# Performance work log

Hardware: AMD Instinct MI355X
Metric: run time of the kernel (lower is better)

Reference implementation:

```python
import jax, jax.numpy as jnp
import numpy as np

B, L, D, DIN, A, V, R = 1024, 100, 256, 704, 128, 32000, 129


def setup_inputs() -> dict:
    key = jax.random.key(0)
    ks = jax.random.split(key, 18)
    s = 0.05
    inp = {
        "x": jax.random.normal(ks[0], (B, DIN), jnp.float32),
        "h0": jax.random.normal(ks[1], (B, D), jnp.float32),
        "c0": jax.random.normal(ks[2], (B, D), jnp.float32),
        "src_enc": jax.random.normal(ks[3], (B, L, D), jnp.float32),
        "src_token_ids": jax.random.randint(ks[4], (B, L), 0, V),
        "W_ih": jax.random.normal(ks[5], (4 * D, DIN), jnp.float32) * s,
        "b_ih": jax.random.normal(ks[6], (4 * D,), jnp.float32) * s,
        "W_hh": jax.random.normal(ks[7], (4 * D, D), jnp.float32) * s,
        "b_hh": jax.random.normal(ks[8], (4 * D,), jnp.float32) * s,
        "W_attn": jax.random.normal(ks[9], (D, D), jnp.float32) * s,
        "W_att_vec": jax.random.normal(ks[10], (A * 2, 2 * D), jnp.float32) * s,
        "W_ptr": jax.random.normal(ks[11], (D, D), jnp.float32) * s,
        "rule_emb": jax.random.normal(ks[12], (R, 128), jnp.float32) * s,
        "W_rule_proj": jax.random.normal(ks[13], (D, 128), jnp.float32) * s,
        "prim_emb": jax.random.normal(ks[14], (V, 128), jnp.float32) * s,
        "W_prim_proj": jax.random.normal(ks[15], (D, 128), jnp.float32) * s,
        "w_gen": jax.random.normal(ks[16], (2, D), jnp.float32) * s,
        "b_gen": jax.random.normal(ks[17], (2,), jnp.float32) * s,
    }
    # W_att_vec maps concat(h, ctx) [2D] -> ATT (=256); keep shape (256, 512)
    inp["W_att_vec"] = inp["W_att_vec"][:256]
    return inp


def reference(x, h0, c0, src_enc, src_token_ids, W_ih, b_ih, W_hh, b_hh,
              W_attn, W_att_vec, W_ptr, rule_emb, W_rule_proj,
              prim_emb, W_prim_proj, w_gen, b_gen):
    # --- LSTMCell (torch gate order i, f, g, o) ---
    gates = x @ W_ih.T + b_ih + h0 @ W_hh.T + b_hh          # [B, 4D]
    i, f, g, o = jnp.split(gates, 4, axis=-1)
    i, f, o = jax.nn.sigmoid(i), jax.nn.sigmoid(f), jax.nn.sigmoid(o)
    c = f * c0 + i * jnp.tanh(g)
    h = o * jnp.tanh(c)                                      # [B, D]

    # --- dot-product attention over source encodings ---
    enc_proj = src_enc @ W_attn.T                            # [B, L, D]
    scores = jnp.einsum('bd,bld->bl', h, enc_proj)
    alpha = jax.nn.softmax(scores, axis=-1)
    ctx = jnp.einsum('bl,bld->bd', alpha, src_enc)
    att = jnp.tanh(jnp.concatenate([h, ctx], axis=-1) @ W_att_vec.T)  # [B, 256]

    # --- apply-rule (production) readout ---
    rule_proj = rule_emb @ W_rule_proj.T                     # [R, 256]
    log_p_rule = jax.nn.log_softmax(att @ rule_proj.T, axis=-1)  # [B, R]

    # --- primitive generation readout ---
    prim_proj = prim_emb @ W_prim_proj.T                     # [V, 256]
    p_gen_prim = jax.nn.softmax(att @ prim_proj.T, axis=-1)  # [B, V]

    # --- pointer network copy distribution over source positions ---
    ptr_scores = jnp.einsum('bld,bd->bl', src_enc @ W_ptr.T, att)
    copy_p = jax.nn.softmax(ptr_scores, axis=-1)             # [B, L]

    # --- gen vs copy gate (softmax over 2, per usage in parse()) ---
    gate = jax.nn.softmax(att @ w_gen.T + b_gen, axis=-1)    # [B, 2]

    # --- combined primitive distribution: gen + scattered copy mass ---
    p_prim = gate[:, :1] * p_gen_prim                        # [B, V]
    copy_mass = gate[:, 1:] * copy_p                         # [B, L]
    bidx = jnp.arange(p_prim.shape[0])[:, None]
    p_prim = p_prim.at[bidx, src_token_ids].add(copy_mass)
    return log_p_rule, p_prim, h, c, att
```

## Files before the change

kernel.cpp:

```cpp
#include <hip/hip_runtime.h>
#include <hip/hip_bf16.h>
#include <math.h>

#define NB   1024
#define LL   100
#define DD   256
#define DINN 704
#define VV   32000
#define RR   129
#define KAV  512
#define ROWU 129

typedef float f32x4 __attribute__((ext_vector_type(4)));
typedef float f32x2 __attribute__((ext_vector_type(2)));
typedef short s16x8 __attribute__((ext_vector_type(8)));
typedef unsigned short u16;
typedef unsigned int u32;

__device__ __forceinline__ float sigf(float x) { return 1.0f / (1.0f + __expf(-x)); }

__device__ __forceinline__ u16 f2bf(float f) {
    u32 u = __float_as_uint(f);
    u += 0x7fffu + ((u >> 16) & 1u);
    return (u16)(u >> 16);
}
__device__ __forceinline__ float bf2f(u16 s) {
    return __uint_as_float(((u32)s) << 16);
}

__global__ __launch_bounds__(256) void k_conv(
    const float* __restrict__ prim_emb, u16* __restrict__ prim_bf,
    const float* __restrict__ W_ih, u16* __restrict__ wih_bf,
    const float* __restrict__ W_hh, u16* __restrict__ whh_bf,
    const float* __restrict__ x, u16* __restrict__ x_bf,
    const float* __restrict__ h0, u16* __restrict__ h0_bf,
    const float* __restrict__ rule_emb, const float* __restrict__ W_rule_proj,
    float* __restrict__ rpT)
{
    __shared__ float re_s[128];
    const int bx = blockIdx.x, t = threadIdx.x;

    const float* src; u16* dst; int off;
    if (bx < 2000)      { src = prim_emb; dst = prim_bf; off = bx * 2048; }
    else if (bx < 2352) { src = W_ih;  dst = wih_bf; off = (bx - 2000) * 2048; }
    else if (bx < 2480) { src = W_hh;  dst = whh_bf; off = (bx - 2352) * 2048; }
    else if (bx < 2832) { src = x;     dst = x_bf;   off = (bx - 2480) * 2048; }
    else                { src = h0;    dst = h0_bf;  off = (bx - 2832) * 2048; }

    if (bx < RR && t < 128) re_s[t] = rule_emb[bx * 128 + t];

    int i = off + t * 8;
    f32x4 a = *reinterpret_cast<const f32x4*>(&src[i]);
    f32x4 b = *reinterpret_cast<const f32x4*>(&src[i + 4]);
    s16x8 r;
    r[0] = (short)f2bf(a[0]); r[1] = (short)f2bf(a[1]);
    r[2] = (short)f2bf(a[2]); r[3] = (short)f2bf(a[3]);
    r[4] = (short)f2bf(b[0]); r[5] = (short)f2bf(b[1]);
    r[6] = (short)f2bf(b[2]); r[7] = (short)f2bf(b[3]);
    *reinterpret_cast<s16x8*>(&dst[i]) = r;

    if (bx < RR) {
        __syncthreads();
        float acc = 0.f;
        const float* __restrict__ wr = &W_rule_proj[t * 128];
#pragma unroll 8
        for (int k = 0; k < 128; k += 4) {
            f32x4 w4 = *reinterpret_cast<const f32x4*>(&wr[k]);
            acc += w4[0] * re_s[k] + w4[1] * re_s[k + 1]
                 + w4[2] * re_s[k + 2] + w4[3] * re_s[k + 3];
        }
        rpT[t * 192 + bx] = acc;
    }
}

__global__ __launch_bounds__(256) void k_lstm(
    const u16* __restrict__ x_bf, const u16* __restrict__ h0_bf,
    const float* __restrict__ c0,
    const u16* __restrict__ wih_bf, const u16* __restrict__ whh_bf,
    const float* __restrict__ b_ih, const float* __restrict__ b_hh,
    float* __restrict__ out_h, float* __restrict__ out_c)
{
    const int t = threadIdx.x;
    const int lane = t & 63, w = t >> 6;
    const int lm = lane & 15, lq = lane >> 4;
    const int dg = blockIdx.x;
    const int row0 = blockIdx.y * 128 + w * 32;
    f32x4 acc[4][2] = {};

    for (int kt = 0; kt < 22; ++kt) {
        const int ko = kt * 32 + lq * 8;
        s16x8 bfr[4], afr[2];
#pragma unroll
        for (int mg = 0; mg < 4; ++mg)
            bfr[mg] = *reinterpret_cast<const s16x8*>(
                &wih_bf[(mg * 256 + dg * 16 + lm) * DINN + ko]);
#pragma unroll
        for (int ng = 0; ng < 2; ++ng)
            afr[ng] = *reinterpret_cast<const s16x8*>(
                &x_bf[(row0 + ng * 16 + lm) * DINN + ko]);
#pragma unroll
        for (int mg = 0; mg < 4; ++mg)
#pragma unroll
            for (int ng = 0; ng < 2; ++ng)
                acc[mg][ng] = __builtin_amdgcn_mfma_f32_16x16x32_bf16(
                    bfr[mg], afr[ng], acc[mg][ng], 0, 0, 0);
    }
    for (int kt = 0; kt < 8; ++kt) {
        const int ko = kt * 32 + lq * 8;
        s16x8 bfr[4], afr[2];
#pragma unroll
        for (int mg = 0; mg < 4; ++mg)
            bfr[mg] = *reinterpret_cast<const s16x8*>(
                &whh_bf[(mg * 256 + dg * 16 + lm) * DD + ko]);
#pragma unroll
        for (int ng = 0; ng < 2; ++ng)
            afr[ng] = *reinterpret_cast<const s16x8*>(
                &h0_bf[(row0 + ng * 16 + lm) * DD + ko]);
#pragma unroll
        for (int mg = 0; mg < 4; ++mg)
#pragma unroll
            for (int ng = 0; ng < 2; ++ng)
                acc[mg][ng] = __builtin_amdgcn_mfma_f32_16x16x32_bf16(
                    bfr[mg], afr[ng], acc[mg][ng], 0, 0, 0);
    }

    const int dc = dg * 16 + lq * 4;
    f32x4 bi[4];
#pragma unroll
    for (int mg = 0; mg < 4; ++mg) {
        f32x4 a4 = *reinterpret_cast<const f32x4*>(&b_ih[mg * 256 + dc]);
        f32x4 b4 = *reinterpret_cast<const f32x4*>(&b_hh[mg * 256 + dc]);
        bi[mg][0] = a4[0] + b4[0]; bi[mg][1] = a4[1] + b4[1];
        bi[mg][2] = a4[2] + b4[2]; bi[mg][3] = a4[3] + b4[3];
    }
#pragma unroll
    for (int ng = 0; ng < 2; ++ng) {
        const int row = row0 + ng * 16 + lm;
        f32x4 c4 = *reinterpret_cast<const f32x4*>(&c0[row * DD + dc]);
        f32x4 h4, cc4;
#pragma unroll
        for (int r = 0; r < 4; ++r) {
            float iv = acc[0][ng][r] + bi[0][r];
            float fv = acc[1][ng][r] + bi[1][r];
            float gv = acc[2][ng][r] + bi[2][r];
            float ov = acc[3][ng][r] + bi[3][r];
            float cc = sigf(fv) * c4[r] + sigf(iv) * tanhf(gv);
            cc4[r] = cc;
            h4[r] = sigf(ov) * tanhf(cc);
        }
        *reinterpret_cast<f32x4*>(&out_c[row * DD + dc]) = cc4;
        *reinterpret_cast<f32x4*>(&out_h[row * DD + dc]) = h4;
    }
}

__global__ __launch_bounds__(256) void k_hw(
    const float* __restrict__ h, const float* __restrict__ W_attn, float* __restrict__ hW)
{
    __shared__ __align__(16) float As[16][36];
    __shared__ __align__(16) float Bs[16][68];
    const int t = threadIdx.x;
    const int row0 = blockIdx.x * 32;
    const int col0 = blockIdx.y * 64;
    const int tr = t >> 4, tc = t & 15;
    float acc[2][4] = {};
    for (int kt = 0; kt < 16; ++kt) {
        __syncthreads();
#pragma unroll
        for (int p = 0; p < 2; ++p) {
            int e = t + p * 256;
            int r = e >> 4, kk = e & 15;
            As[kk][r] = h[(row0 + r) * DD + kt * 16 + kk];
        }
#pragma unroll
        for (int p = 0; p < 4; ++p) {
            int e = t + p * 256;
            int kk = e >> 6, c = e & 63;
            Bs[kk][c] = W_attn[(kt * 16 + kk) * DD + col0 + c];
        }
        __syncthreads();
#pragma unroll
        for (int kk = 0; kk < 16; ++kk) {
            float a0 = As[kk][tr * 2], a1 = As[kk][tr * 2 + 1];
            f32x4 b = *reinterpret_cast<const f32x4*>(&Bs[kk][tc * 4]);
#pragma unroll
            for (int i = 0; i < 4; ++i) {
                acc[0][i] = fmaf(a0, b[i], acc[0][i]);
                acc[1][i] = fmaf(a1, b[i], acc[1][i]);
            }
        }
    }
#pragma unroll
    for (int j = 0; j < 2; ++j) {
        f32x4 v;
#pragma unroll
        for (int i = 0; i < 4; ++i) v[i] = acc[j][i];
        *reinterpret_cast<f32x4*>(&hW[(row0 + tr * 2 + j) * DD + col0 + tc * 4]) = v;
    }
}

__global__ __launch_bounds__(256, 2) void k_attn2(
    const float* __restrict__ src_enc, const float* __restrict__ hW,
    float* __restrict__ ctx_out)
{
    __shared__ u32 enc_u[LL * ROWU];
    __shared__ __align__(16) float part[4][DD];
    __shared__ __align__(16) float hw_s[DD];
    __shared__ float sc_s[LL];
    __shared__ float al_s[LL];

    const int b = blockIdx.x, t = threadIdx.x;
    const int lane = t & 63, w = t >> 6;
    const float* __restrict__ enc = src_enc + (size_t)b * LL * DD;

    hw_s[t] = hW[b * DD + t];

#pragma unroll
    for (int p = 0; p < 25; ++p) {
        int q = p * 256 + t;
        int l = q >> 6, dq = q & 63;
        f32x4 ev = *reinterpret_cast<const f32x4*>(&enc[l * DD + dq * 4]);
        u32 w0 = (u32)f2bf(ev[0]) | ((u32)f2bf(ev[1]) << 16);
        u32 w1 = (u32)f2bf(ev[2]) | ((u32)f2bf(ev[3]) << 16);
        enc_u[l * ROWU + dq * 2]     = w0;
        enc_u[l * ROWU + dq * 2 + 1] = w1;
    }
    __syncthreads();

    {
        const int sl = ((w >> 1) << 6) + lane;
        float sp = 0.f;
        if (sl < LL) {
            const u32* __restrict__ rp = enc_u + sl * ROWU + ((w & 1) << 6);
            const float* __restrict__ hp = hw_s + ((w & 1) << 7);
#pragma unroll 32
            for (int k = 0; k < 64; ++k) {
                u32 v = rp[k];
                sp = fmaf(bf2f((u16)v),         hp[2 * k],     sp);
                sp = fmaf(bf2f((u16)(v >> 16)), hp[2 * k + 1], sp);
            }
        }
        part[w][lane] = sp;
    }
    __syncthreads();
    if (t < LL) sc_s[t] = part[(t >> 6) << 1][t & 63] + part[((t >> 6) << 1) + 1][t & 63];
    __syncthreads();

    if (w == 0) {
        float v0 = sc_s[lane];
        float v1 = (lane + 64 < LL) ? sc_s[lane + 64] : -1e30f;
        float m = fmaxf(v0, v1);
#pragma unroll
        for (int s = 1; s < 64; s <<= 1) m = fmaxf(m, __shfl_xor(m, s));
        float e0 = __expf(v0 - m);
        float e1 = (lane + 64 < LL) ? __expf(v1 - m) : 0.f;
        float ssum = e0 + e1;
#pragma unroll
        for (int s = 1; s < 64; s <<= 1) ssum += __shfl_xor(ssum, s);
        float inv = 1.f / ssum;
        al_s[lane] = e0 * inv;
        if (lane + 64 < LL) al_s[lane + 64] = e1 * inv;
    }
    __syncthreads();

    {
        const int l0 = w * 25;
        float c0 = 0.f, c1 = 0.f, c2 = 0.f, c3 = 0.f;
#pragma unroll
        for (int li = 0; li < 25; ++li) {
            int l = l0 + li;
            float a = al_s[l];
            u32 v0 = enc_u[l * ROWU + lane * 2];
            u32 v1 = enc_u[l * ROWU + lane * 2 + 1];
            c0 = fmaf(a, bf2f((u16)v0), c0);
            c1 = fmaf(a, bf2f((u16)(v0 >> 16)), c1);
            c2 = fmaf(a, bf2f((u16)v1), c2);
            c3 = fmaf(a, bf2f((u16)(v1 >> 16)), c3);
        }
        f32x4 p; p[0] = c0; p[1] = c1; p[2] = c2; p[3] = c3;
        *reinterpret_cast<f32x4*>(&part[w][lane * 4]) = p;
    }
    __syncthreads();
    ctx_out[b * DD + t] = (part[0][t] + part[1][t]) + (part[2][t] + part[3][t]);
}

__global__ __launch_bounds__(256) void k_att(
    const float* __restrict__ h, const float* __restrict__ ctx,
    const float* __restrict__ W_att_vec, float* __restrict__ att_out)
{
    __shared__ __align__(16) float As[16][36];
    __shared__ __align__(16) float Bs[16][68];
    const int t = threadIdx.x;
    const int row0 = blockIdx.x * 32;
    const int col0 = blockIdx.y * 64;
    const int tr = t >> 4, tc = t & 15;
    float acc[2][4] = {};
    for (int kt = 0; kt < 32; ++kt) {
        const float* __restrict__ Asrc = (kt < 16) ? h : ctx;
        int kb = (kt < 16) ? kt * 16 : (kt - 16) * 16;
        int kg = kt * 16;
        __syncthreads();
#pragma unroll
        for (int p = 0; p < 2; ++p) {
            int e = t + p * 256;
            int r = e >> 4, kk = e & 15;
            As[kk][r] = Asrc[(row0 + r) * DD + kb + kk];
        }
#pragma unroll
        for (int p = 0; p < 4; ++p) {
            int e = t + p * 256;
            int r = e >> 4, kk = e & 15;
            Bs[kk][r] = W_att_vec[(col0 + r) * KAV + kg + kk];
        }
        __syncthreads();
#pragma unroll
        for (int kk = 0; kk < 16; ++kk) {
            float a0 = As[kk][tr * 2], a1 = As[kk][tr * 2 + 1];
            f32x4 b = *reinterpret_cast<const f32x4*>(&Bs[kk][tc * 4]);
#pragma unroll
            for (int i = 0; i < 4; ++i) {
                acc[0][i] = fmaf(a0, b[i], acc[0][i]);
                acc[1][i] = fmaf(a1, b[i], acc[1][i]);
            }
        }
    }
#pragma unroll
    for (int j = 0; j < 2; ++j)
#pragma unroll
        for (int i = 0; i < 4; ++i)
            att_out[(row0 + tr * 2 + j) * DD + col0 + tc * 4 + i] = tanhf(acc[j][i]);
}

__global__ __launch_bounds__(256) void k_ptrproj(
    const float* __restrict__ att, const float* __restrict__ W_ptr,
    const float* __restrict__ W_prim_proj, const float* __restrict__ rpT,
    float* __restrict__ atw, u16* __restrict__ att_bf, float* __restrict__ rl)
{
    __shared__ __align__(16) float As[16][36];
    __shared__ __align__(16) float Bs[16][68];
    const int t = threadIdx.x;
    const int row0 = blockIdx.x * 32;
    const int col0 = blockIdx.y * 64;
    const int tr = t >> 4, tc = t & 15;
    float acc[2][4] = {};
    for (int kt = 0; kt < 16; ++kt) {
        __syncthreads();
#pragma unroll
        for (int p = 0; p < 2; ++p) {
            int e = t + p * 256;
            int r = e >> 4, kk = e & 15;
            As[kk][r] = att[(row0 + r) * DD + kt * 16 + kk];
        }
#pragma unroll
        for (int p = 0; p < 4; ++p) {
            int e = t + p * 256;
            int kk = e >> 6, c = e & 63;
            float bv;
            if (col0 < 256)      bv = W_ptr[(kt * 16 + kk) * DD + col0 + c];
            else if (col0 < 384) bv = W_prim_proj[(kt * 16 + kk) * 128 + (col0 - 256) + c];
            else {
                int rc = col0 - 384 + c;
                bv = (rc < RR) ? rpT[(kt * 16 + kk) * 192 + rc] : 0.f;
            }
            Bs[kk][c] = bv;
        }
        __syncthreads();
#pragma unroll
        for (int kk = 0; kk < 16; ++kk) {
            float a0 = As[kk][tr * 2], a1 = As[kk][tr * 2 + 1];
            f32x4 b = *reinterpret_cast<const f32x4*>(&Bs[kk][tc * 4]);
#pragma unroll
            for (int i = 0; i < 4; ++i) {
                acc[0][i] = fmaf(a0, b[i], acc[0][i]);
                acc[1][i] = fmaf(a1, b[i], acc[1][i]);
            }
        }
    }
    if (col0 < 256) {
#pragma unroll
        for (int j = 0; j < 2; ++j) {
            f32x4 v;
#pragma unroll
            for (int i = 0; i < 4; ++i) v[i] = acc[j][i];
            *reinterpret_cast<f32x4*>(&atw[(row0 + tr * 2 + j) * DD + col0 + tc * 4]) = v;
        }
    } else if (col0 < 384) {
#pragma unroll
        for (int j = 0; j < 2; ++j)
#pragma unroll
            for (int i = 0; i < 4; ++i)
                att_bf[(row0 + tr * 2 + j) * 128 + (col0 - 256) + tc * 4 + i] = f2bf(acc[j][i]);
    } else {
#pragma unroll
        for (int j = 0; j < 2; ++j)
#pragma unroll
            for (int i = 0; i < 4; ++i) {
                int rc = col0 - 384 + tc * 4 + i;
                if (rc < RR) rl[(row0 + tr * 2 + j) * 132 + rc] = acc[j][i];
            }
    }
}

__global__ __launch_bounds__(256) void k_fin(
    const float* __restrict__ rl, const float* __restrict__ att,
    const float* __restrict__ w_gen, const float* __restrict__ b_gen,
    float* __restrict__ log_p_rule, float* __restrict__ gate0_ws,
    float* __restrict__ gate1_ws)
{
    const int w = threadIdx.x >> 6, lane = threadIdx.x & 63;
    const int b = blockIdx.x * 4 + w;

    float v0 = rl[b * 132 + lane];
    float v1 = rl[b * 132 + 64 + lane];
    float v2 = (lane == 0) ? rl[b * 132 + 128] : -1e30f;
    float m = fmaxf(fmaxf(v0, v1), v2);
#pragma unroll
    for (int s = 1; s < 64; s <<= 1) m = fmaxf(m, __shfl_xor(m, s));
    float ssum = __expf(v0 - m) + __expf(v1 - m) + ((lane == 0) ? __expf(v2 - m) : 0.f);
#pragma unroll
    for (int s = 1; s < 64; s <<= 1) ssum += __shfl_xor(ssum, s);
    float ls = m + logf(ssum);
    log_p_rule[b * RR + lane] = v0 - ls;
    log_p_rule[b * RR + 64 + lane] = v1 - ls;
    if (lane == 0) log_p_rule[b * RR + 128] = v2 - ls;

    f32x4 a4 = *reinterpret_cast<const f32x4*>(&att[b * DD + lane * 4]);
    f32x4 g0 = *reinterpret_cast<const f32x4*>(&w_gen[lane * 4]);
    f32x4 g1 = *reinterpret_cast<const f32x4*>(&w_gen[DD + lane * 4]);
    float p0 = a4[0] * g0[0] + a4[1] * g0[1] + a4[2] * g0[2] + a4[3] * g0[3];
    float p1 = a4[0] * g1[0] + a4[1] * g1[1] + a4[2] * g1[2] + a4[3] * g1[3];
#pragma unroll
    for (int s = 1; s < 64; s <<= 1) { p0 += __shfl_xor(p0, s); p1 += __shfl_xor(p1, s); }
    if (lane == 0) {
        float ga = p0 + b_gen[0], gb = p1 + b_gen[1];
        float gm = fmaxf(ga, gb);
        float ea = __expf(ga - gm), eb = __expf(gb - gm);
        gate0_ws[b] = ea / (ea + eb);
        gate1_ws[b] = eb / (ea + eb);
    }
}

__global__ __launch_bounds__(256) void k_ptr2(
    const float* __restrict__ src_enc, const float* __restrict__ atw,
    const float* __restrict__ gate1_ws, float* __restrict__ copy_mass)
{
    __shared__ float sc_s[LL];
    const int b = blockIdx.x, t = threadIdx.x;
    const int lane = t & 63, w = t >> 6;
    const float* __restrict__ enc = src_enc + (size_t)b * LL * DD;
    f32x4 aw4 = *reinterpret_cast<const f32x4*>(&atw[b * DD + lane * 4]);

    for (int l = w; l < LL; l += 4) {
        f32x4 ev = *reinterpret_cast<const f32x4*>(&enc[l * DD + lane * 4]);
        float pr = aw4[0] * ev[0] + aw4[1] * ev[1] + aw4[2] * ev[2] + aw4[3] * ev[3];
#pragma unroll
        for (int m = 1; m < 64; m <<= 1) pr += __shfl_xor(pr, m);
        if (lane == 0) sc_s[l] = pr;
    }
    __syncthreads();
    if (w == 0) {
        float gate1 = gate1_ws[b];
        float v0 = sc_s[lane];
        float v1 = (lane + 64 < LL) ? sc_s[lane + 64] : -1e30f;
        float m = fmaxf(v0, v1);
#pragma unroll
        for (int s = 1; s < 64; s <<= 1) m = fmaxf(m, __shfl_xor(m, s));
        float ee0 = __expf(v0 - m);
        float ee1 = (lane + 64 < LL) ? __expf(v1 - m) : 0.f;
        float ssum = ee0 + ee1;
#pragma unroll
        for (int s = 1; s < 64; s <<= 1) ssum += __shfl_xor(ssum, s);
        float inv = 1.f / ssum;
        copy_mass[b * LL + lane] = gate1 * ee0 * inv;
        if (lane + 64 < LL) copy_mass[b * LL + lane + 64] = gate1 * ee1 * inv;
    }
}

template <int PASS>
__global__ __launch_bounds__(256) void k_prim(
    const u16* __restrict__ att_bf, const u16* __restrict__ prim_bf,
    const float* __restrict__ coef, float* __restrict__ stats, float* __restrict__ p_prim)
{
    const int t = threadIdx.x;
    const int lane = t & 63, w = t >> 6;
    const int lm = lane & 15, lq = lane >> 4;
    const int colbase = blockIdx.x * 128 + (w & 1) * 64;
    const int chunk = colbase >> 6;
    const int rowblk = blockIdx.y * 256;

    s16x8 pfr[4][4];
#pragma unroll
    for (int kg = 0; kg < 4; ++kg)
#pragma unroll
        for (int mg = 0; mg < 4; ++mg)
            pfr[kg][mg] = *reinterpret_cast<const s16x8*>(
                &prim_bf[(size_t)(colbase + mg * 16 + lm) * 128 + kg * 32 + lq * 8]);

    for (int it = 0; it < 2; ++it) {
        const int rowbase = rowblk + it * 128 + (w >> 1) * 64;
        f32x4 acc[4][4] = {};
#pragma unroll
        for (int kg = 0; kg < 4; ++kg) {
            s16x8 afr[4];
#pragma unroll
            for (int ng = 0; ng < 4; ++ng)
                afr[ng] = *reinterpret_cast<const s16x8*>(
                    &att_bf[(rowbase + ng * 16 + lm) * 128 + kg * 32 + lq * 8]);
#pragma unroll
            for (int mg = 0; mg < 4; ++mg)
#pragma unroll
                for (int ng = 0; ng < 4; ++ng)
                    acc[mg][ng] = __builtin_amdgcn_mfma_f32_16x16x32_bf16(
                        pfr[kg][mg], afr[ng], acc[mg][ng], 0, 0, 0);
        }
        if (PASS == 0) {
#pragma unroll
            for (int ng = 0; ng < 4; ++ng) {
                float se = 0.f;
#pragma unroll
                for (int mg = 0; mg < 4; ++mg)
                    se += __expf(acc[mg][ng][0]) + __expf(acc[mg][ng][1])
                        + __expf(acc[mg][ng][2]) + __expf(acc[mg][ng][3]);
                se += __shfl_xor(se, 16);
                se += __shfl_xor(se, 32);
                if (lq == 0)
                    stats[chunk * NB + rowbase + ng * 16 + lm] = se;
            }
        } else {
#pragma unroll
            for (int ng = 0; ng < 4; ++ng) {
                const int arow = rowbase + ng * 16 + lm;
                const float cf = coef[arow];
                float* __restrict__ dst = &p_prim[(size_t)arow * VV + colbase + lq * 4];
#pragma unroll
                for (int mg = 0; mg < 4; ++mg) {
                    f32x4 v;
                    v[0] = cf * __expf(acc[mg][ng][0]);
                    v[1] = cf * __expf(acc[mg][ng][1]);
                    v[2] = cf * __expf(acc[mg][ng][2]);
                    v[3] = cf * __expf(acc[mg][ng][3]);
                    *reinterpret_cast<f32x4*>(&dst[mg * 16]) = v;
                }
            }
        }
    }
}

__global__ __launch_bounds__(256) void k_combine(
    const float* __restrict__ stats, const float* __restrict__ gate0_ws,
    float* __restrict__ coef)
{
    const int row = blockIdx.x * 256 + threadIdx.x;
    float s0 = 0.f, s1 = 0.f, s2 = 0.f, s3 = 0.f;
    for (int c = 0; c < 500; c += 4) {
        s0 += stats[(c)     * NB + row];
        s1 += stats[(c + 1) * NB + row];
        s2 += stats[(c + 2) * NB + row];
        s3 += stats[(c + 3) * NB + row];
    }
    coef[row] = gate0_ws[row] / ((s0 + s1) + (s2 + s3));
}

__global__ __launch_bounds__(256) void k_scatter(
    const int* __restrict__ tok, const float* __restrict__ copy_mass, float* __restrict__ p_prim)
{
    int i = blockIdx.x * 256 + threadIdx.x;
    if (i >= NB * LL) return;
    int b = i / LL;
    atomicAdd(&p_prim[(size_t)b * VV + tok[i]], copy_mass[i]);
}

extern "C" void kernel_launch(void* const* d_in, const int* in_sizes, int n_in,
                              void* d_out, int out_size, void* d_ws, size_t ws_size,
                              hipStream_t stream)
{
    const float* x         = (const float*)d_in[0];
    const float* h0        = (const float*)d_in[1];
    const float* c0        = (const float*)d_in[2];
    const float* src_enc   = (const float*)d_in[3];
    const int*   tok       = (const int*)  d_in[4];
    const float* W_ih      = (const float*)d_in[5];
    const float* b_ih      = (const float*)d_in[6];
    const float* W_hh      = (const float*)d_in[7];
    const float* b_hh      = (const float*)d_in[8];
    const float* W_attn    = (const float*)d_in[9];
    const float* W_att_vec = (const float*)d_in[10];
    const float* W_ptr     = (const float*)d_in[11];
    const float* rule_emb  = (const float*)d_in[12];
    const float* W_rule_pr = (const float*)d_in[13];
    const float* prim_emb  = (const float*)d_in[14];
    const float* W_prim_pr = (const float*)d_in[15];
    const float* w_gen     = (const float*)d_in[16];
    const float* b_gen     = (const float*)d_in[17];

    float* out    = (float*)d_out;
    float* o_logp = out;
    float* o_pp   = out + 1024 * 129;
    float* o_h    = o_pp + (size_t)1024 * 32000;
    float* o_c    = o_h + 1024 * 256;
    float* o_att  = o_c + 1024 * 256;

    float* wsf      = (float*)d_ws;
    float* ws_rpT   = wsf;
    float* ws_rl    = ws_rpT   + 49152;
    float* ws_gate0 = ws_rl    + 135168;
    float* ws_gate1 = ws_gate0 + 1024;
    float* ws_cm    = ws_gate1 + 1024;
    float* ws_coef  = ws_cm    + 102400;
    float* ws_hw    = ws_coef  + 1024;
    float* ws_ctx   = ws_hw    + 262144;
    float* ws_atw   = ws_ctx   + 262144;
    float* ws_stats = ws_atw   + 262144;
    u16*   ub       = (u16*)(ws_stats + 512000);
    u16*   ws_attbf = ub;
    u16*   ws_primbf= ws_attbf + 131072;
    u16*   ws_xb    = ws_primbf + 4096000;
    u16*   ws_h0b   = ws_xb    + 720896;
    u16*   ws_wihb  = ws_h0b   + 262144;
    u16*   ws_whhb  = ws_wihb  + 720896;

    k_conv<<<dim3(2960), 256, 0, stream>>>(prim_emb, ws_primbf, W_ih, ws_wihb,
                                           W_hh, ws_whhb, x, ws_xb, h0, ws_h0b,
                                           rule_emb, W_rule_pr, ws_rpT);
    k_lstm<<<dim3(16, 8), 256, 0, stream>>>(ws_xb, ws_h0b, c0, ws_wihb, ws_whhb,
                                            b_ih, b_hh, o_h, o_c);
    k_hw<<<dim3(32, 4), 256, 0, stream>>>(o_h, W_attn, ws_hw);
    k_attn2<<<dim3(1024), 256, 0, stream>>>(src_enc, ws_hw, ws_ctx);
    k_att<<<dim3(32, 4), 256, 0, stream>>>(o_h, ws_ctx, W_att_vec, o_att);
    k_ptrproj<<<dim3(32, 9), 256, 0, stream>>>(o_att, W_ptr, W_prim_pr, ws_rpT,
                                               ws_atw, ws_attbf, ws_rl);
    k_fin<<<dim3(256), 256, 0, stream>>>(ws_rl, o_att, w_gen, b_gen,
                                         o_logp, ws_gate0, ws_gate1);
    k_ptr2<<<dim3(1024), 256, 0, stream>>>(src_enc, ws_atw, ws_gate1, ws_cm);
    k_prim<0><<<dim3(250, 4), 256, 0, stream>>>(ws_attbf, ws_primbf, nullptr, ws_stats, nullptr);
    k_combine<<<dim3(4), 256, 0, stream>>>(ws_stats, ws_gate0, ws_coef);
    k_prim<1><<<dim3(250, 4), 256, 0, stream>>>(ws_attbf, ws_primbf, ws_coef, nullptr, o_pp);
    k_scatter<<<dim3(400), 256, 0, stream>>>(tok, ws_cm, o_pp);
}
```

Measured before the change: 235.0 us.

## Merge fin, pointer softmax and first prim pass into one launch

Three independent kernels (rule log-softmax plus gate, pointer copy softmax, and the first-pass vocabulary exp-sum) are merged into one kernel dispatched by block index. This lets them run concurrently and removes two launch boundaries. To break the dependency of the pointer branch on the gate, the gate1 multiply moves into the scatter kernel. The cost is a larger, register-heavier merged kernel whose block branches differ in occupancy needs.

```diff
diff --git a/kernel.cpp b/kernel.cpp
--- a/kernel.cpp
+++ b/kernel.cpp
@@ -12,7 +12,6 @@
 #define ROWU 129
 
 typedef float f32x4 __attribute__((ext_vector_type(4)));
-typedef float f32x2 __attribute__((ext_vector_type(2)));
 typedef short s16x8 __attribute__((ext_vector_type(8)));
 typedef unsigned short u16;
 typedef unsigned int u32;
@@ -400,119 +399,117 @@
     }
 }
 
-__global__ __launch_bounds__(256) void k_fin(
+__global__ __launch_bounds__(256) void k_back(
     const float* __restrict__ rl, const float* __restrict__ att,
     const float* __restrict__ w_gen, const float* __restrict__ b_gen,
     float* __restrict__ log_p_rule, float* __restrict__ gate0_ws,
-    float* __restrict__ gate1_ws)
-{
-    const int w = threadIdx.x >> 6, lane = threadIdx.x & 63;
-    const int b = blockIdx.x * 4 + w;
-
-    float v0 = rl[b * 132 + lane];
-    float v1 = rl[b * 132 + 64 + lane];
-    float v2 = (lane == 0) ? rl[b * 132 + 128] : -1e30f;
-    float m = fmaxf(fmaxf(v0, v1), v2);
-#pragma unroll
-    for (int s = 1; s < 64; s <<= 1) m = fmaxf(m, __shfl_xor(m, s));
-    float ssum = __expf(v0 - m) + __expf(v1 - m) + ((lane == 0) ? __expf(v2 - m) : 0.f);
-#pragma unroll
-    for (int s = 1; s < 64; s <<= 1) ssum += __shfl_xor(ssum, s);
-    float ls = m + logf(ssum);
-    log_p_rule[b * RR + lane] = v0 - ls;
-    log_p_rule[b * RR + 64 + lane] = v1 - ls;
-    if (lane == 0) log_p_rule[b * RR + 128] = v2 - ls;
-
-    f32x4 a4 = *reinterpret_cast<const f32x4*>(&att[b * DD + lane * 4]);
-    f32x4 g0 = *reinterpret_cast<const f32x4*>(&w_gen[lane * 4]);
-    f32x4 g1 = *reinterpret_cast<const f32x4*>(&w_gen[DD + lane * 4]);
-    float p0 = a4[0] * g0[0] + a4[1] * g0[1] + a4[2] * g0[2] + a4[3] * g0[3];
-    float p1 = a4[0] * g1[0] + a4[1] * g1[1] + a4[2] * g1[2] + a4[3] * g1[3];
-#pragma unroll
-    for (int s = 1; s < 64; s <<= 1) { p0 += __shfl_xor(p0, s); p1 += __shfl_xor(p1, s); }
-    if (lane == 0) {
-        float ga = p0 + b_gen[0], gb = p1 + b_gen[1];
-        float gm = fmaxf(ga, gb);
-        float ea = __expf(ga - gm), eb = __expf(gb - gm);
-        gate0_ws[b] = ea / (ea + eb);
-        gate1_ws[b] = eb / (ea + eb);
-    }
-}
-
-__global__ __launch_bounds__(256) void k_ptr2(
+    float* __restrict__ gate1_ws,
     const float* __restrict__ src_enc, const float* __restrict__ atw,
-    const float* __restrict__ gate1_ws, float* __restrict__ copy_mass)
+    float* __restrict__ copy_mass,
+    const u16* __restrict__ att_bf, const u16* __restrict__ prim_bf,
+    float* __restrict__ stats)
 {
     __shared__ float sc_s[LL];
-    const int b = blockIdx.x, t = threadIdx.x;
+    const int bx = blockIdx.x, t = threadIdx.x;
     const int lane = t & 63, w = t >> 6;
-    const float* __restrict__ enc = src_enc + (size_t)b * LL * DD;
-    f32x4 aw4 = *reinterpret_cast<const f32x4*>(&atw[b * DD + lane * 4]);
-
-    for (int l = w; l < LL; l += 4) {
-        f32x4 ev = *reinterpret_cast<const f32x4*>(&enc[l * DD + lane * 4]);
-        float pr = aw4[0] * ev[0] + aw4[1] * ev[1] + aw4[2] * ev[2] + aw4[3] * ev[3];
-#pragma unroll
-        for (int m = 1; m < 64; m <<= 1) pr += __shfl_xor(pr, m);
-        if (lane == 0) sc_s[l] = pr;
-    }
-    __syncthreads();
-    if (w == 0) {
-        float gate1 = gate1_ws[b];
-        float v0 = sc_s[lane];
-        float v1 = (lane + 64 < LL) ? sc_s[lane + 64] : -1e30f;
-        float m = fmaxf(v0, v1);
+
+    if (bx < 256) {
+        const int b = bx * 4 + w;
+        float v0 = rl[b * 132 + lane];
+        float v1 = rl[b * 132 + 64 + lane];
+        float v2 = (lane == 0) ? rl[b * 132 + 128] : -1e30f;
+        float m = fmaxf(fmaxf(v0, v1), v2);
 #pragma unroll
         for (int s = 1; s < 64; s <<= 1) m = fmaxf(m, __shfl_xor(m, s));
-        float ee0 = __expf(v0 - m);
-        float ee1 = (lane + 64 < LL) ? __expf(v1 - m) : 0.f;
-        float ssum = ee0 + ee1;
+        float ssum = __expf(v0 - m) + __expf(v1 - m) + ((lane == 0) ? __expf(v2 - m) : 0.f);
 #pragma unroll
         for (int s = 1; s < 64; s <<= 1) ssum += __shfl_xor(ssum, s);
-        float inv = 1.f / ssum;
-        copy_mass[b * LL + lane] = gate1 * ee0 * inv;
-        if (lane + 64 < LL) copy_mass[b * LL + lane + 64] = gate1 * ee1 * inv;
-    }
-}
-
-template <int PASS>
-__global__ __launch_bounds__(256) void k_prim(
-    const u16* __restrict__ att_bf, const u16* __restrict__ prim_bf,
-    const float* __restrict__ coef, float* __restrict__ stats, float* __restrict__ p_prim)
-{
-    const int t = threadIdx.x;
-    const int lane = t & 63, w = t >> 6;
-    const int lm = lane & 15, lq = lane >> 4;
-    const int colbase = blockIdx.x * 128 + (w & 1) * 64;
-    const int chunk = colbase >> 6;
-    const int rowblk = blockIdx.y * 256;
-
-    s16x8 pfr[4][4];
-#pragma unroll
-    for (int kg = 0; kg < 4; ++kg)
-#pragma unroll
-        for (int mg = 0; mg < 4; ++mg)
-            pfr[kg][mg] = *reinterpret_cast<const s16x8*>(
-                &prim_bf[(size_t)(colbase + mg * 16 + lm) * 128 + kg * 32 + lq * 8]);
-
-    for (int it = 0; it < 2; ++it) {
-        const int rowbase = rowblk + it * 128 + (w >> 1) * 64;
-        f32x4 acc[4][4] = {};
-#pragma unroll
-        for (int kg = 0; kg < 4; ++kg) {
-            s16x8 afr[4];
-#pragma unroll
-            for (int ng = 0; ng < 4; ++ng)
-                afr[ng] = *reinterpret_cast<const s16x8*>(
-                    &att_bf[(rowbase + ng * 16 + lm) * 128 + kg * 32 + lq * 8]);
+        float ls = m + logf(ssum);
+        log_p_rule[b * RR + lane] = v0 - ls;
+        log_p_rule[b * RR + 64 + lane] = v1 - ls;
+        if (lane == 0) log_p_rule[b * RR + 128] = v2 - ls;
+
+        f32x4 a4 = *reinterpret_cast<const f32x4*>(&att[b * DD + lane * 4]);
+        f32x4 g0 = *reinterpret_cast<const f32x4*>(&w_gen[lane * 4]);
+        f32x4 g1 = *reinterpret_cast<const f32x4*>(&w_gen[DD + lane * 4]);
+        float p0 = a4[0] * g0[0] + a4[1] * g0[1] + a4[2] * g0[2] + a4[3] * g0[3];
+        float p1 = a4[0] * g1[0] + a4[1] * g1[1] + a4[2] * g1[2] + a4[3] * g1[3];
+#pragma unroll
+        for (int s = 1; s < 64; s <<= 1) { p0 += __shfl_xor(p0, s); p1 += __shfl_xor(p1, s); }
+        if (lane == 0) {
+            float ga = p0 + b_gen[0], gb = p1 + b_gen[1];
+            float gm = fmaxf(ga, gb);
+            float ea = __expf(ga - gm), eb = __expf(gb - gm);
+            gate0_ws[b] = ea / (ea + eb);
+            gate1_ws[b] = eb / (ea + eb);
+        }
+        return;
+    }
+
+    if (bx < 1280) {
+        const int b = bx - 256;
+        const float* __restrict__ enc = src_enc + (size_t)b * LL * DD;
+        f32x4 aw4 = *reinterpret_cast<const f32x4*>(&atw[b * DD + lane * 4]);
+
+        for (int l = w; l < LL; l += 4) {
+            f32x4 ev = *reinterpret_cast<const f32x4*>(&enc[l * DD + lane * 4]);
+            float pr = aw4[0] * ev[0] + aw4[1] * ev[1] + aw4[2] * ev[2] + aw4[3] * ev[3];
+#pragma unroll
+            for (int m = 1; m < 64; m <<= 1) pr += __shfl_xor(pr, m);
+            if (lane == 0) sc_s[l] = pr;
+        }
+        __syncthreads();
+        if (w == 0) {
+            float v0 = sc_s[lane];
+            float v1 = (lane + 64 < LL) ? sc_s[lane + 64] : -1e30f;
+            float m = fmaxf(v0, v1);
+#pragma unroll
+            for (int s = 1; s < 64; s <<= 1) m = fmaxf(m, __shfl_xor(m, s));
+            float ee0 = __expf(v0 - m);
+            float ee1 = (lane + 64 < LL) ? __expf(v1 - m) : 0.f;
+            float ssum = ee0 + ee1;
+#pragma unroll
+            for (int s = 1; s < 64; s <<= 1) ssum += __shfl_xor(ssum, s);
+            float inv = 1.f / ssum;
+            copy_mass[b * LL + lane] = ee0 * inv;
+            if (lane + 64 < LL) copy_mass[b * LL + lane + 64] = ee1 * inv;
+        }
+        return;
+    }
+
+    {
+        const int cb = bx - 1280;
+        const int colb = cb % 250, rowblk = cb / 250;
+        const int lm = lane & 15, lq = lane >> 4;
+        const int colbase = colb * 128 + (w & 1) * 64;
+        const int chunk = colbase >> 6;
+        const int rowblk_g = rowblk * 256;
+
+        s16x8 pfr[4][4];
+#pragma unroll
+        for (int kg = 0; kg < 4; ++kg)
 #pragma unroll
             for (int mg = 0; mg < 4; ++mg)
+                pfr[kg][mg] = *reinterpret_cast<const s16x8*>(
+                    &prim_bf[(size_t)(colbase + mg * 16 + lm) * 128 + kg * 32 + lq * 8]);
+
+        for (int it = 0; it < 2; ++it) {
+            const int rowbase = rowblk_g + it * 128 + (w >> 1) * 64;
+            f32x4 acc[4][4] = {};
+#pragma unroll
+            for (int kg = 0; kg < 4; ++kg) {
+                s16x8 afr[4];
 #pragma unroll
                 for (int ng = 0; ng < 4; ++ng)
-                    acc[mg][ng] = __builtin_amdgcn_mfma_f32_16x16x32_bf16(
-                        pfr[kg][mg], afr[ng], acc[mg][ng], 0, 0, 0);
-        }
-        if (PASS == 0) {
+                    afr[ng] = *reinterpret_cast<const s16x8*>(
+                        &att_bf[(rowbase + ng * 16 + lm) * 128 + kg * 32 + lq * 8]);
+#pragma unroll
+                for (int mg = 0; mg < 4; ++mg)
+#pragma unroll
+                    for (int ng = 0; ng < 4; ++ng)
+                        acc[mg][ng] = __builtin_amdgcn_mfma_f32_16x16x32_bf16(
+                            pfr[kg][mg], afr[ng], acc[mg][ng], 0, 0, 0);
+            }
 #pragma unroll
             for (int ng = 0; ng < 4; ++ng) {
                 float se = 0.f;
@@ -525,21 +522,58 @@
                 if (lq == 0)
                     stats[chunk * NB + rowbase + ng * 16 + lm] = se;
             }
-        } else {
-#pragma unroll
-            for (int ng = 0; ng < 4; ++ng) {
-                const int arow = rowbase + ng * 16 + lm;
-                const float cf = coef[arow];
-                float* __restrict__ dst = &p_prim[(size_t)arow * VV + colbase + lq * 4];
-#pragma unroll
-                for (int mg = 0; mg < 4; ++mg) {
-                    f32x4 v;
-                    v[0] = cf * __expf(acc[mg][ng][0]);
-                    v[1] = cf * __expf(acc[mg][ng][1]);
-                    v[2] = cf * __expf(acc[mg][ng][2]);
-                    v[3] = cf * __expf(acc[mg][ng][3]);
-                    *reinterpret_cast<f32x4*>(&dst[mg * 16]) = v;
-                }
+        }
+    }
+}
+
+__global__ __launch_bounds__(256) void k_prim1(
+    const u16* __restrict__ att_bf, const u16* __restrict__ prim_bf,
+    const float* __restrict__ coef, float* __restrict__ p_prim)
+{
+    const int t = threadIdx.x;
+    const int lane = t & 63, w = t >> 6;
+    const int lm = lane & 15, lq = lane >> 4;
+    const int colbase = blockIdx.x * 128 + (w & 1) * 64;
+    const int rowblk = blockIdx.y * 256;
+
+    s16x8 pfr[4][4];
+#pragma unroll
+    for (int kg = 0; kg < 4; ++kg)
+#pragma unroll
+        for (int mg = 0; mg < 4; ++mg)
+            pfr[kg][mg] = *reinterpret_cast<const s16x8*>(
+                &prim_bf[(size_t)(colbase + mg * 16 + lm) * 128 + kg * 32 + lq * 8]);
+
+    for (int it = 0; it < 2; ++it) {
+        const int rowbase = rowblk + it * 128 + (w >> 1) * 64;
+        f32x4 acc[4][4] = {};
+#pragma unroll
+        for (int kg = 0; kg < 4; ++kg) {
+            s16x8 afr[4];
+#pragma unroll
+            for (int ng = 0; ng < 4; ++ng)
+                afr[ng] = *reinterpret_cast<const s16x8*>(
+                    &att_bf[(rowbase + ng * 16 + lm) * 128 + kg * 32 + lq * 8]);
+#pragma unroll
+            for (int mg = 0; mg < 4; ++mg)
+#pragma unroll
+                for (int ng = 0; ng < 4; ++ng)
+                    acc[mg][ng] = __builtin_amdgcn_mfma_f32_16x16x32_bf16(
+                        pfr[kg][mg], afr[ng], acc[mg][ng], 0, 0, 0);
+        }
+#pragma unroll
+        for (int ng = 0; ng < 4; ++ng) {
+            const int arow = rowbase + ng * 16 + lm;
+            const float cf = coef[arow];
+            float* __restrict__ dst = &p_prim[(size_t)arow * VV + colbase + lq * 4];
+#pragma unroll
+            for (int mg = 0; mg < 4; ++mg) {
+                f32x4 v;
+                v[0] = cf * __expf(acc[mg][ng][0]);
+                v[1] = cf * __expf(acc[mg][ng][1]);
+                v[2] = cf * __expf(acc[mg][ng][2]);
+                v[3] = cf * __expf(acc[mg][ng][3]);
+                *reinterpret_cast<f32x4*>(&dst[mg * 16]) = v;
             }
         }
     }
@@ -561,12 +595,13 @@
 }
 
 __global__ __launch_bounds__(256) void k_scatter(
-    const int* __restrict__ tok, const float* __restrict__ copy_mass, float* __restrict__ p_prim)
+    const int* __restrict__ tok, const float* __restrict__ copy_mass,
+    const float* __restrict__ gate1_ws, float* __restrict__ p_prim)
 {
     int i = blockIdx.x * 256 + threadIdx.x;
     if (i >= NB * LL) return;
     int b = i / LL;
-    atomicAdd(&p_prim[(size_t)b * VV + tok[i]], copy_mass[i]);
+    atomicAdd(&p_prim[(size_t)b * VV + tok[i]], gate1_ws[b] * copy_mass[i]);
 }
 
 extern "C" void kernel_launch(void* const* d_in, const int* in_sizes, int n_in,
@@ -628,11 +663,11 @@
     k_att<<<dim3(32, 4), 256, 0, stream>>>(o_h, ws_ctx, W_att_vec, o_att);
     k_ptrproj<<<dim3(32, 9), 256, 0, stream>>>(o_att, W_ptr, W_prim_pr, ws_rpT,
                                                ws_atw, ws_attbf, ws_rl);
-    k_fin<<<dim3(256), 256, 0, stream>>>(ws_rl, o_att, w_gen, b_gen,
-                                         o_logp, ws_gate0, ws_gate1);
-    k_ptr2<<<dim3(1024), 256, 0, stream>>>(src_enc, ws_atw, ws_gate1, ws_cm);
-    k_prim<0><<<dim3(250, 4), 256, 0, stream>>>(ws_attbf, ws_primbf, nullptr, ws_stats, nullptr);
+    k_back<<<dim3(2280), 256, 0, stream>>>(ws_rl, o_att, w_gen, b_gen,
+                                           o_logp, ws_gate0, ws_gate1,
+                                           src_enc, ws_atw, ws_cm,
+                                           ws_attbf, ws_primbf, ws_stats);
     k_combine<<<dim3(4), 256, 0, stream>>>(ws_stats, ws_gate0, ws_coef);
-    k_prim<1><<<dim3(250, 4), 256, 0, stream>>>(ws_attbf, ws_primbf, ws_coef, nullptr, o_pp);
-    k_scatter<<<dim3(400), 256, 0, stream>>>(tok, ws_cm, o_pp);
-}
+    k_prim1<<<dim3(250, 4), 256, 0, stream>>>(ws_attbf, ws_primbf, ws_coef, o_pp);
+    k_scatter<<<dim3(400), 256, 0, stream>>>(tok, ws_cm, ws_gate1, o_pp);
+}
```

Result: slower. 240.7 us (+2.5%).
